# Kernel tuning notes

Hardware: AMD Instinct MI355X
Metric: run time of the kernel (lower is better)

Reference implementation:

```python
import math
import jax, jax.numpy as jnp
import numpy as np

B, S, HID = 2, 2048, 3072
NH, HD = 32, 96            # num_heads, head_dim; num_kv_heads == num_heads (n_rep = 1)
OP = NH * HD + 2 * (NH * HD)  # 9216


def _rope_tables(seq_len, head_dim, theta=10000.0):
    inv_freq = 1.0 / (theta ** (np.arange(0, head_dim, 2, dtype=np.float32) / head_dim))
    t = np.arange(seq_len, dtype=np.float32)
    freqs = np.outer(t, inv_freq)                      # [S, HD/2]
    emb = np.concatenate([freqs, freqs], axis=-1)      # [S, HD]
    return jnp.asarray(np.cos(emb)), jnp.asarray(np.sin(emb))


def setup_inputs() -> dict:
    key = jax.random.key(0)
    k1, k2, k3 = jax.random.split(key, 3)
    hidden_states = jax.random.normal(k1, (B, S, HID), dtype=jnp.float32)
    cos, sin = _rope_tables(S, HD)
    # additive causal mask [B, 1, S, S]
    neg = jnp.finfo(jnp.float32).min
    causal = jnp.where(jnp.tril(jnp.ones((S, S), dtype=bool)), 0.0, neg)
    attention_mask = jnp.broadcast_to(causal[None, None], (B, 1, S, S)).astype(jnp.float32)
    Wqkv = jax.random.normal(k2, (HID, OP), dtype=jnp.float32) * (HID ** -0.5)
    Wo = jax.random.normal(k3, (NH * HD, HID), dtype=jnp.float32) * ((NH * HD) ** -0.5)
    return {"hidden_states": hidden_states, "cos": cos, "sin": sin,
            "attention_mask": attention_mask, "Wqkv": Wqkv, "Wo": Wo}


def _rotate_half(x):
    x1, x2 = jnp.split(x, 2, axis=-1)
    return jnp.concatenate([-x2, x1], axis=-1)


def reference(hidden_states, cos, sin, attention_mask, Wqkv, Wo):
    bsz, q_len, _ = hidden_states.shape
    qkv = hidden_states @ Wqkv                                    # [B,S,OP]
    q, k, v = jnp.split(qkv, [NH * HD, 2 * NH * HD], axis=-1)
    # [B,S,H*D] -> [B,H,S,D]
    to_bhsd = lambda t: t.reshape(bsz, q_len, NH, HD).transpose(0, 2, 1, 3)
    q, k, v = to_bhsd(q), to_bhsd(k), to_bhsd(v)
    c = cos[None, None]                                           # [1,1,S,D]
    s = sin[None, None]
    q = q * c + _rotate_half(q) * s
    k = k * c + _rotate_half(k) * s
    # num_key_value_groups == 1, so repeat_kv is identity.
    scores = jnp.einsum('bhqd,bhkd->bhqk', q, k) / math.sqrt(HD)  # [B,H,S,S]
    scores = scores + attention_mask
    attn = jax.nn.softmax(scores.astype(jnp.float32), axis=-1).astype(v.dtype)
    # dropout p=0.0 / eval -> identity
    out = jnp.einsum('bhqk,bhkd->bhqd', attn, v)                  # [B,H,S,D]
    out = out.transpose(0, 2, 1, 3).reshape(bsz, q_len, NH * HD)
    return out @ Wo                                               # [B,S,HID]
```

## Files before the change

kernel.cpp:

```cpp
#include <hip/hip_runtime.h>

typedef __bf16  bf16x8 __attribute__((ext_vector_type(8)));
typedef float   f32x4  __attribute__((ext_vector_type(4)));
typedef float   f32x16 __attribute__((ext_vector_type(16)));
typedef short   i16x8  __attribute__((ext_vector_type(8)));
typedef unsigned short u16x4 __attribute__((ext_vector_type(4)));
typedef unsigned int   u32x4 __attribute__((ext_vector_type(4)));

__device__ __forceinline__ float bf2f(unsigned short u) {
    union { unsigned int i; float f; } v; v.i = ((unsigned int)u) << 16; return v.f;
}
__device__ __forceinline__ unsigned short f2bf(float f) {
    union { float f; unsigned int i; } v; v.f = f;
    unsigned int r = v.i + 0x7FFFu + ((v.i >> 16) & 1u);
    return (unsigned short)(r >> 16);
}
__device__ __forceinline__ unsigned packbf(float lo, float hi) {
    return (unsigned)f2bf(lo) | ((unsigned)f2bf(hi) << 16);
}
__device__ __forceinline__ void gload_lds16(const void* g, void* l) {
    __builtin_amdgcn_global_load_lds(
        (const __attribute__((address_space(1))) void*)g,
        (__attribute__((address_space(3))) void*)l, 16, 0, 0);
}
__device__ __forceinline__ void pswap(unsigned &x, unsigned &y) {
#if __has_builtin(__builtin_amdgcn_permlane32_swap)
    auto r = __builtin_amdgcn_permlane32_swap((int)x, (int)y, false, false);
    x = (unsigned)r[0]; y = (unsigned)r[1];
#else
    unsigned nx = (threadIdx.x & 32) ? (unsigned)__shfl_xor((int)y, 32) : x;
    unsigned ny = (threadIdx.x & 32) ? y : (unsigned)__shfl_xor((int)x, 32);
    x = nx; y = ny;
#endif
}
__device__ __forceinline__ float partner_f(float v, int hi) {
    unsigned x = __builtin_bit_cast(unsigned, v), y = x;
    pswap(x, y);
    return __builtin_bit_cast(float, hi ? x : y);
}

__global__ __launch_bounds__(256) void cast_f32_bf16(
    const float* __restrict__ in, unsigned short* __restrict__ out, int n8)
{
    int i = blockIdx.x * 256 + threadIdx.x;
    if (i >= n8) return;
    const f32x4* p = (const f32x4*)(in + (long)i * 8);
    f32x4 a = p[0], b = p[1];
    i16x8 o;
    o[0]=(short)f2bf(a[0]); o[1]=(short)f2bf(a[1]); o[2]=(short)f2bf(a[2]); o[3]=(short)f2bf(a[3]);
    o[4]=(short)f2bf(b[0]); o[5]=(short)f2bf(b[1]); o[6]=(short)f2bf(b[2]); o[7]=(short)f2bf(b[3]);
    *(i16x8*)(out + (long)i * 8) = o;
}

__global__ __launch_bounds__(256) void transpose_cast(
    const float* __restrict__ in, unsigned short* __restrict__ out, int R, int C)
{
    __shared__ float tile[64][65];
    int c0 = blockIdx.x * 64, r0 = blockIdx.y * 64;
    int tx = threadIdx.x & 63, ty = threadIdx.x >> 6;
#pragma unroll
    for (int i = 0; i < 64; i += 4)
        tile[ty + i][tx] = in[(long)(r0 + ty + i) * C + c0 + tx];
    __syncthreads();
#pragma unroll
    for (int i = 0; i < 64; i += 4)
        out[(long)(c0 + ty + i) * R + r0 + tx] = f2bf(tile[tx][ty + i]);
}

template <int MODE>
__global__ __launch_bounds__(256) void gemm_bt(
    const unsigned short* __restrict__ A, const unsigned short* __restrict__ B,
    int K, int N,
    unsigned short* __restrict__ Qo, unsigned short* __restrict__ Ko,
    unsigned short* __restrict__ Vo, float* __restrict__ Cf)
{
    __shared__ unsigned short Al[128 * 64];
    __shared__ unsigned short Bl[128 * 64];
    const int t = threadIdx.x;
    const int w = t >> 6, l = t & 63, lhi = l >> 4, llo = l & 15;
    const int m0 = blockIdx.x * 128, n0 = blockIdx.y * 128;
    const int wmo = (w >> 1) << 6, wno = (w & 1) << 6;

    const unsigned short* ag[4];
    const unsigned short* bg[4];
#pragma unroll
    for (int i = 0; i < 4; ++i) {
        int j = i * 256 + t;
        int row = j >> 3;
        int c = (j & 7) ^ (row & 7);
        ag[i] = A + (long)(m0 + row) * K + c * 8;
        bg[i] = B + (long)(n0 + row) * K + c * 8;
    }

    f32x4 acc[4][4] = {};
    const int nkt = K >> 6;
    for (int kt = 0; kt < nkt; ++kt) {
        __syncthreads();
#pragma unroll
        for (int i = 0; i < 4; ++i) {
            gload_lds16(ag[i] + kt * 64, &Al[(i * 256 + (w << 6)) * 8]);
            gload_lds16(bg[i] + kt * 64, &Bl[(i * 256 + (w << 6)) * 8]);
        }
        __syncthreads();
#pragma unroll
        for (int kf = 0; kf < 2; ++kf) {
            bf16x8 af[4], bfv[4];
#pragma unroll
            for (int mi = 0; mi < 4; ++mi) {
                int row = wmo + mi * 16 + llo;
                int cc = (kf * 4 + lhi) ^ (row & 7);
                af[mi] = __builtin_bit_cast(bf16x8, *(const i16x8*)&Al[row * 64 + cc * 8]);
            }
#pragma unroll
            for (int ni = 0; ni < 4; ++ni) {
                int row = wno + ni * 16 + llo;
                int cc = (kf * 4 + lhi) ^ (row & 7);
                bfv[ni] = __builtin_bit_cast(bf16x8, *(const i16x8*)&Bl[row * 64 + cc * 8]);
            }
#pragma unroll
            for (int mi = 0; mi < 4; ++mi)
#pragma unroll
                for (int ni = 0; ni < 4; ++ni)
                    acc[mi][ni] = __builtin_amdgcn_mfma_f32_16x16x32_bf16(
                        af[mi], bfv[ni], acc[mi][ni], 0, 0, 0);
        }
    }

#pragma unroll
    for (int mi = 0; mi < 4; ++mi) {
        int s0g = m0 + wmo + mi * 16 + (lhi << 2);
#pragma unroll
        for (int ni = 0; ni < 4; ++ni) {
            int gcol = n0 + wno + ni * 16 + llo;
            if (MODE == 1) {
#pragma unroll
                for (int r = 0; r < 4; ++r)
                    Cf[(long)(s0g + r) * N + gcol] = acc[mi][ni][r];
            } else {
                int seg = gcol / 3072;
                int cc2 = gcol - seg * 3072;
                int h = cc2 / 96, d = cc2 - h * 96;
                int b = s0g >> 11, s = s0g & 2047;
                long bh = (long)((b << 5) + h);
                if (seg == 2) {
                    u16x4 pv;
#pragma unroll
                    for (int r = 0; r < 4; ++r) pv[r] = f2bf(acc[mi][ni][r]);
                    *(u16x4*)(Vo + (bh * 96 + d) * 2048 + s) = pv;
                } else {
                    unsigned short* dst = seg ? Ko : Qo;
#pragma unroll
                    for (int r = 0; r < 4; ++r)
                        dst[(bh * 2048 + s + r) * 96 + d] = f2bf(acc[mi][ni][r]);
                }
            }
        }
    }
}

__global__ __launch_bounds__(256) void rope_kernel(
    unsigned short* __restrict__ Qb, unsigned short* __restrict__ Kb,
    const float* __restrict__ cosT, const float* __restrict__ sinT)
{
    int i = blockIdx.x * 256 + threadIdx.x;
    int d6 = i % 6;
    int sbh = i / 6;
    int s = sbh & 2047;
    long base = (long)sbh * 96 + d6 * 8;
    const f32x4* cp = (const f32x4*)(cosT + s * 96 + d6 * 8);
    const f32x4* sp = (const f32x4*)(sinT + s * 96 + d6 * 8);
    f32x4 c0 = cp[0], c1 = cp[1], s0 = sp[0], s1 = sp[1];
    float cv[8] = {c0[0],c0[1],c0[2],c0[3],c1[0],c1[1],c1[2],c1[3]};
    float sv[8] = {s0[0],s0[1],s0[2],s0[3],s1[0],s1[1],s1[2],s1[3]};
    i16x8 qlo = *(i16x8*)(Qb + base), qhi = *(i16x8*)(Qb + base + 48);
    i16x8 klo = *(i16x8*)(Kb + base), khi = *(i16x8*)(Kb + base + 48);
    i16x8 qlo2, qhi2, klo2, khi2;
#pragma unroll
    for (int j = 0; j < 8; ++j) {
        float ql = bf2f((unsigned short)qlo[j]), qh = bf2f((unsigned short)qhi[j]);
        float kl = bf2f((unsigned short)klo[j]), kh = bf2f((unsigned short)khi[j]);
        qlo2[j] = (short)f2bf(ql * cv[j] - qh * sv[j]);
        qhi2[j] = (short)f2bf(qh * cv[j] + ql * sv[j]);
        klo2[j] = (short)f2bf(kl * cv[j] - kh * sv[j]);
        khi2[j] = (short)f2bf(kh * cv[j] + kl * sv[j]);
    }
    *(i16x8*)(Qb + base) = qlo2; *(i16x8*)(Qb + base + 48) = qhi2;
    *(i16x8*)(Kb + base) = klo2; *(i16x8*)(Kb + base + 48) = khi2;
}

__global__ __launch_bounds__(256, 2) void attn_fwd(
    const unsigned short* __restrict__ Q, const unsigned short* __restrict__ Kt,
    const unsigned short* __restrict__ Vg, unsigned short* __restrict__ O)
{
    __shared__ __align__(16) unsigned short Kl[2][64 * 128];
    __shared__ __align__(16) unsigned short Vl[2][96 * 64];
    const int t = threadIdx.x;
    const int w = t >> 6, l = t & 63;
    const int l31 = l & 31, hi = l >> 5, l7 = l & 7;
    const int bh = blockIdx.x;
    const int qb = 7 - (int)blockIdx.y;
    const int q0b = qb << 8;
    const int nkv = 4 * qb + 4;
    const int kd = 4 * qb + w;
    constexpr float C2 = 0.14724450f;

    const unsigned short* Kg  = Kt + (long)bh * 2048 * 96;
    const unsigned short* Vgb = Vg + (long)bh * 96 * 2048;

#define STAGE_KV(buf, tile)                                                        \
    {                                                                              \
        _Pragma("unroll")                                                          \
        for (int i_ = 0; i_ < 4; ++i_) {                                           \
            int row_ = (w << 4) + (i_ << 2) + (l >> 4);                            \
            gload_lds16(Kg + ((long)(tile) * 64 + row_) * 96 +                     \
                            (((l & 15) ^ (row_ & 7)) << 3),                        \
                        &Kl[buf][((w << 4) + (i_ << 2)) << 7]);                    \
        }                                                                          \
        _Pragma("unroll")                                                          \
        for (int i_ = 0; i_ < 3; ++i_) {                                           \
            int row_ = w * 24 + (i_ << 3) + (l >> 3);                              \
            gload_lds16(Vgb + (long)row_ * 2048 + (tile) * 64 +                    \
                            ((l7 ^ (row_ & 7)) << 3),                              \
                        &Vl[buf][(w * 24 + (i_ << 3)) << 6]);                      \
        }                                                                          \
    }

    bf16x8 qf[2][6];
#pragma unroll
    for (int qs = 0; qs < 2; ++qs) {
        const unsigned short* qp =
            Q + ((long)bh * 2048 + q0b + (w << 6) + (qs << 5) + l31) * 96 + (hi << 3);
#pragma unroll
        for (int ks = 0; ks < 6; ++ks)
            qf[qs][ks] = __builtin_bit_cast(bf16x8, *(const i16x8*)(qp + ks * 16));
    }

    f32x16 oa[2][3] = {};
    float m_r[2] = {-1e30f, -1e30f};
    float l_r[2] = {0.f, 0.f};

    STAGE_KV(0, 0);
    __syncthreads();
    STAGE_KV(1, 1);

    for (int kt = 0; kt < nkv; ++kt) {
        const int cb = kt & 1;
        if (kt <= kd) {
            bf16x8 pf[2][4];
#pragma unroll
            for (int qs = 0; qs < 2; ++qs) {
                f32x16 s0 = {}, s1 = {};
#pragma unroll
                for (int ks = 0; ks < 6; ++ks) {
                    bf16x8 k0 = __builtin_bit_cast(bf16x8, *(const i16x8*)
                        &Kl[cb][(l31 << 7) + ((((ks << 1) + hi) ^ l7) << 3)]);
                    bf16x8 k1 = __builtin_bit_cast(bf16x8, *(const i16x8*)
                        &Kl[cb][((32 + l31) << 7) + ((((ks << 1) + hi) ^ l7) << 3)]);
                    s0 = __builtin_amdgcn_mfma_f32_32x32x16_bf16(k0, qf[qs][ks], s0, 0, 0, 0);
                    s1 = __builtin_amdgcn_mfma_f32_32x32x16_bf16(k1, qf[qs][ks], s1, 0, 0, 0);
                }
                if (kt == kd) {
                    const int ql = (qs << 5) + l31;
#pragma unroll
                    for (int r = 0; r < 16; ++r) {
                        int kvl = (r & 3) + ((r >> 2) << 3) + (hi << 2);
                        if (kvl > ql)      s0[r] = -1e30f;
                        if (kvl + 32 > ql) s1[r] = -1e30f;
                    }
                }
                float px = s0[0];
#pragma unroll
                for (int r = 1; r < 16; ++r) px = fmaxf(px, s0[r]);
#pragma unroll
                for (int r = 0; r < 16; ++r) px = fmaxf(px, s1[r]);
                px = fmaxf(px, partner_f(px, hi));
                if (__any(px > m_r[qs] + 54.0f)) {
                    float mnew = fmaxf(m_r[qs], px);
                    float scl = exp2f((m_r[qs] - mnew) * C2);
                    l_r[qs] *= scl;
#pragma unroll
                    for (int tt = 0; tt < 3; ++tt)
#pragma unroll
                        for (int r = 0; r < 16; ++r) oa[qs][tt][r] *= scl;
                    m_r[qs] = mnew;
                }
                const float mC = m_r[qs] * C2;
                f32x16 p0, p1;
                float ls = 0.f;
#pragma unroll
                for (int r = 0; r < 16; ++r) {
                    p0[r] = exp2f(fmaf(s0[r], C2, -mC));
                    p1[r] = exp2f(fmaf(s1[r], C2, -mC));
                    ls += p0[r] + p1[r];
                }
                l_r[qs] += ls;
#pragma unroll
                for (int s = 0; s < 4; ++s) {
                    const f32x16& pv = (s >= 2) ? p1 : p0;
                    const int bb = (s & 1) << 3;
                    unsigned d0 = packbf(pv[bb + 0], pv[bb + 1]);
                    unsigned d2 = packbf(pv[bb + 4], pv[bb + 5]);
                    pswap(d0, d2);
                    unsigned d1 = packbf(pv[bb + 2], pv[bb + 3]);
                    unsigned d3 = packbf(pv[bb + 6], pv[bb + 7]);
                    pswap(d1, d3);
                    pf[qs][s] = __builtin_bit_cast(bf16x8, (u32x4){d0, d1, d2, d3});
                }
            }
#pragma unroll
            for (int s = 0; s < 4; ++s) {
#pragma unroll
                for (int tt = 0; tt < 3; ++tt) {
                    bf16x8 vf = __builtin_bit_cast(bf16x8, *(const i16x8*)
                        &Vl[cb][((tt << 5) + l31) * 64 + ((((s << 1) + hi) ^ l7) << 3)]);
                    oa[0][tt] = __builtin_amdgcn_mfma_f32_32x32x16_bf16(vf, pf[0][s], oa[0][tt], 0, 0, 0);
                    oa[1][tt] = __builtin_amdgcn_mfma_f32_32x32x16_bf16(vf, pf[1][s], oa[1][tt], 0, 0, 0);
                }
            }
        }
        __syncthreads();
        if (kt + 2 < nkv) STAGE_KV(cb, kt + 2);
    }
#undef STAGE_KV

    const int b = bh >> 5, h = bh & 31;
#pragma unroll
    for (int qs = 0; qs < 2; ++qs) {
        float lt = l_r[qs] + partner_f(l_r[qs], hi);
        float inv = 1.0f / lt;
        const int qg = q0b + (w << 6) + (qs << 5) + l31;
        unsigned short* ob = O + ((long)(b * 2048 + qg)) * 3072 + h * 96;
#pragma unroll
        for (int tt = 0; tt < 3; ++tt)
#pragma unroll
            for (int qd = 0; qd < 4; ++qd) {
                u16x4 o4;
#pragma unroll
                for (int j = 0; j < 4; ++j)
                    o4[j] = f2bf(oa[qs][tt][(qd << 2) + j] * inv);
                *(u16x4*)(ob + (tt << 5) + (qd << 3) + (hi << 2)) = o4;
            }
    }
}

extern "C" void kernel_launch(void* const* d_in, const int* in_sizes, int n_in,
                              void* d_out, int out_size, void* d_ws, size_t ws_size,
                              hipStream_t stream) {
    const float* hidden = (const float*)d_in[0];
    const float* cosT   = (const float*)d_in[1];
    const float* sinT   = (const float*)d_in[2];
    const float* Wqkv   = (const float*)d_in[4];
    const float* Wo     = (const float*)d_in[5];
    float* out = (float*)d_out;

    char* ws = (char*)d_ws;
    unsigned short* Ah  = (unsigned short*)ws;
    unsigned short* WqT = (unsigned short*)(ws + 25165824);
    unsigned short* Qb  = (unsigned short*)(ws + 25165824 + 56623104);
    unsigned short* Kb  = Qb + 12582912;
    unsigned short* Vb  = Kb + 12582912;

    cast_f32_bf16<<<6144, 256, 0, stream>>>(hidden, Ah, 1572864);
    transpose_cast<<<dim3(144, 48), 256, 0, stream>>>(Wqkv, WqT, 3072, 9216);
    gemm_bt<0><<<dim3(32, 72), 256, 0, stream>>>(Ah, WqT, 3072, 9216, Qb, Kb, Vb, nullptr);
    transpose_cast<<<dim3(48, 48), 256, 0, stream>>>(Wo, WqT, 3072, 3072);
    rope_kernel<<<3072, 256, 0, stream>>>(Qb, Kb, cosT, sinT);
    attn_fwd<<<dim3(64, 8), 256, 0, stream>>>(Qb, Kb, Vb, Ah);
    gemm_bt<1><<<dim3(32, 24), 256, 0, stream>>>(Ah, WqT, 3072, 3072,
                                                 nullptr, nullptr, nullptr, out);
}
```

Before: 572.0 us.

## Pair causal query blocks per workgroup and triple-buffer KV with explicit waitcnt

Each attention workgroup now handles two query blocks (qb and 7-qb), so the causal work per block is balanced and the grid is halved to 256 blocks. KV staging moves from double to triple buffering, with manual vmcnt waits and raw barriers replacing __syncthreads, so two tiles are in flight while one is being computed. The QK loop is reordered so each K fragment feeds both query sub-tiles, and setprio raises priority around the MFMA sections. Occupancy is cut to one block per CU because of the larger LDS and register footprint, and the hand-written waitcnt counts depend on the exact number of loads STAGE_KV issues.

```diff
diff --git a/kernel.cpp b/kernel.cpp
--- a/kernel.cpp
+++ b/kernel.cpp
@@ -188,20 +188,16 @@
     *(i16x8*)(Kb + base) = klo2; *(i16x8*)(Kb + base + 48) = khi2;
 }
 
-__global__ __launch_bounds__(256, 2) void attn_fwd(
+__global__ __launch_bounds__(256, 1) void attn_fwd(
     const unsigned short* __restrict__ Q, const unsigned short* __restrict__ Kt,
     const unsigned short* __restrict__ Vg, unsigned short* __restrict__ O)
 {
-    __shared__ __align__(16) unsigned short Kl[2][64 * 128];
-    __shared__ __align__(16) unsigned short Vl[2][96 * 64];
+    __shared__ __align__(16) unsigned short Kl[3][64 * 128];
+    __shared__ __align__(16) unsigned short Vl[3][96 * 64];
     const int t = threadIdx.x;
     const int w = t >> 6, l = t & 63;
     const int l31 = l & 31, hi = l >> 5, l7 = l & 7;
     const int bh = blockIdx.x;
-    const int qb = 7 - (int)blockIdx.y;
-    const int q0b = qb << 8;
-    const int nkv = 4 * qb + 4;
-    const int kd = 4 * qb + w;
     constexpr float C2 = 0.14724450f;
 
     const unsigned short* Kg  = Kt + (long)bh * 2048 * 96;
@@ -225,122 +221,147 @@
         }                                                                          \
     }
 
-    bf16x8 qf[2][6];
-#pragma unroll
-    for (int qs = 0; qs < 2; ++qs) {
-        const unsigned short* qp =
-            Q + ((long)bh * 2048 + q0b + (w << 6) + (qs << 5) + l31) * 96 + (hi << 3);
-#pragma unroll
-        for (int ks = 0; ks < 6; ++ks)
-            qf[qs][ks] = __builtin_bit_cast(bf16x8, *(const i16x8*)(qp + ks * 16));
-    }
-
-    f32x16 oa[2][3] = {};
-    float m_r[2] = {-1e30f, -1e30f};
-    float l_r[2] = {0.f, 0.f};
-
-    STAGE_KV(0, 0);
-    __syncthreads();
-    STAGE_KV(1, 1);
-
-    for (int kt = 0; kt < nkv; ++kt) {
-        const int cb = kt & 1;
-        if (kt <= kd) {
-            bf16x8 pf[2][4];
-#pragma unroll
-            for (int qs = 0; qs < 2; ++qs) {
-                f32x16 s0 = {}, s1 = {};
+    const int b = bh >> 5, h = bh & 31;
+
+    for (int pass = 0; pass < 2; ++pass) {
+        const int qb = pass ? 7 - (int)blockIdx.y : (int)blockIdx.y;
+        const int q0b = qb << 8;
+        const int nkv = 4 * qb + 4;
+        const int kd = 4 * qb + w;
+
+        bf16x8 qf[2][6];
+#pragma unroll
+        for (int qs = 0; qs < 2; ++qs) {
+            const unsigned short* qp =
+                Q + ((long)bh * 2048 + q0b + (w << 6) + (qs << 5) + l31) * 96 + (hi << 3);
+#pragma unroll
+            for (int ks = 0; ks < 6; ++ks)
+                qf[qs][ks] = __builtin_bit_cast(bf16x8, *(const i16x8*)(qp + ks * 16));
+        }
+
+        f32x16 oa[2][3] = {};
+        float m_r[2] = {-1e30f, -1e30f};
+        float l_r[2] = {0.f, 0.f};
+
+        STAGE_KV(0, 0);
+        STAGE_KV(1, 1);
+        STAGE_KV(2, 2);
+
+        int cb = 0;
+        for (int kt = 0; kt < nkv; ++kt) {
+            const int rem = nkv - 1 - kt;
+            if (rem >= 2)      asm volatile("s_waitcnt vmcnt(14)" ::: "memory");
+            else if (rem == 1) asm volatile("s_waitcnt vmcnt(7)"  ::: "memory");
+            else               asm volatile("s_waitcnt vmcnt(0)"  ::: "memory");
+            __builtin_amdgcn_s_barrier();
+
+            if (kt <= kd) {
+                f32x16 s0[2] = {}, s1[2] = {};
+                __builtin_amdgcn_s_setprio(1);
 #pragma unroll
                 for (int ks = 0; ks < 6; ++ks) {
                     bf16x8 k0 = __builtin_bit_cast(bf16x8, *(const i16x8*)
                         &Kl[cb][(l31 << 7) + ((((ks << 1) + hi) ^ l7) << 3)]);
                     bf16x8 k1 = __builtin_bit_cast(bf16x8, *(const i16x8*)
                         &Kl[cb][((32 + l31) << 7) + ((((ks << 1) + hi) ^ l7) << 3)]);
-                    s0 = __builtin_amdgcn_mfma_f32_32x32x16_bf16(k0, qf[qs][ks], s0, 0, 0, 0);
-                    s1 = __builtin_amdgcn_mfma_f32_32x32x16_bf16(k1, qf[qs][ks], s1, 0, 0, 0);
-                }
-                if (kt == kd) {
-                    const int ql = (qs << 5) + l31;
+#pragma unroll
+                    for (int qs = 0; qs < 2; ++qs) {
+                        s0[qs] = __builtin_amdgcn_mfma_f32_32x32x16_bf16(k0, qf[qs][ks], s0[qs], 0, 0, 0);
+                        s1[qs] = __builtin_amdgcn_mfma_f32_32x32x16_bf16(k1, qf[qs][ks], s1[qs], 0, 0, 0);
+                    }
+                }
+                __builtin_amdgcn_s_setprio(0);
+
+                bf16x8 pf[2][4];
+#pragma unroll
+                for (int qs = 0; qs < 2; ++qs) {
+                    if (kt == kd) {
+                        const int ql = (qs << 5) + l31;
+#pragma unroll
+                        for (int r = 0; r < 16; ++r) {
+                            int kvl = (r & 3) + ((r >> 2) << 3) + (hi << 2);
+                            if (kvl > ql)      s0[qs][r] = -1e30f;
+                            if (kvl + 32 > ql) s1[qs][r] = -1e30f;
+                        }
+                    }
+                    float px = s0[qs][0];
+#pragma unroll
+                    for (int r = 1; r < 16; ++r) px = fmaxf(px, s0[qs][r]);
+#pragma unroll
+                    for (int r = 0; r < 16; ++r) px = fmaxf(px, s1[qs][r]);
+                    px = fmaxf(px, partner_f(px, hi));
+                    if (__any(px > m_r[qs] + 54.0f)) {
+                        float mnew = fmaxf(m_r[qs], px);
+                        float scl = exp2f((m_r[qs] - mnew) * C2);
+                        l_r[qs] *= scl;
+#pragma unroll
+                        for (int tt = 0; tt < 3; ++tt)
+#pragma unroll
+                            for (int r = 0; r < 16; ++r) oa[qs][tt][r] *= scl;
+                        m_r[qs] = mnew;
+                    }
+                    const float mC = m_r[qs] * C2;
+                    f32x16 p0, p1;
+                    float ls = 0.f;
 #pragma unroll
                     for (int r = 0; r < 16; ++r) {
-                        int kvl = (r & 3) + ((r >> 2) << 3) + (hi << 2);
-                        if (kvl > ql)      s0[r] = -1e30f;
-                        if (kvl + 32 > ql) s1[r] = -1e30f;
-                    }
-                }
-                float px = s0[0];
-#pragma unroll
-                for (int r = 1; r < 16; ++r) px = fmaxf(px, s0[r]);
-#pragma unroll
-                for (int r = 0; r < 16; ++r) px = fmaxf(px, s1[r]);
-                px = fmaxf(px, partner_f(px, hi));
-                if (__any(px > m_r[qs] + 54.0f)) {
-                    float mnew = fmaxf(m_r[qs], px);
-                    float scl = exp2f((m_r[qs] - mnew) * C2);
-                    l_r[qs] *= scl;
-#pragma unroll
-                    for (int tt = 0; tt < 3; ++tt)
-#pragma unroll
-                        for (int r = 0; r < 16; ++r) oa[qs][tt][r] *= scl;
-                    m_r[qs] = mnew;
-                }
-                const float mC = m_r[qs] * C2;
-                f32x16 p0, p1;
-                float ls = 0.f;
-#pragma unroll
-                for (int r = 0; r < 16; ++r) {
-                    p0[r] = exp2f(fmaf(s0[r], C2, -mC));
-                    p1[r] = exp2f(fmaf(s1[r], C2, -mC));
-                    ls += p0[r] + p1[r];
-                }
-                l_r[qs] += ls;
+                        p0[r] = exp2f(fmaf(s0[qs][r], C2, -mC));
+                        p1[r] = exp2f(fmaf(s1[qs][r], C2, -mC));
+                        ls += p0[r] + p1[r];
+                    }
+                    l_r[qs] += ls;
+#pragma unroll
+                    for (int s = 0; s < 4; ++s) {
+                        const f32x16& pv = (s >= 2) ? p1 : p0;
+                        const int bb = (s & 1) << 3;
+                        unsigned d0 = packbf(pv[bb + 0], pv[bb + 1]);
+                        unsigned d2 = packbf(pv[bb + 4], pv[bb + 5]);
+                        pswap(d0, d2);
+                        unsigned d1 = packbf(pv[bb + 2], pv[bb + 3]);
+                        unsigned d3 = packbf(pv[bb + 6], pv[bb + 7]);
+                        pswap(d1, d3);
+                        pf[qs][s] = __builtin_bit_cast(bf16x8, (u32x4){d0, d1, d2, d3});
+                    }
+                }
+                __builtin_amdgcn_s_setprio(1);
 #pragma unroll
                 for (int s = 0; s < 4; ++s) {
-                    const f32x16& pv = (s >= 2) ? p1 : p0;
-                    const int bb = (s & 1) << 3;
-                    unsigned d0 = packbf(pv[bb + 0], pv[bb + 1]);
-                    unsigned d2 = packbf(pv[bb + 4], pv[bb + 5]);
-                    pswap(d0, d2);
-                    unsigned d1 = packbf(pv[bb + 2], pv[bb + 3]);
-                    unsigned d3 = packbf(pv[bb + 6], pv[bb + 7]);
-                    pswap(d1, d3);
-                    pf[qs][s] = __builtin_bit_cast(bf16x8, (u32x4){d0, d1, d2, d3});
-                }
+#pragma unroll
+                    for (int tt = 0; tt < 3; ++tt) {
+                        bf16x8 vf = __builtin_bit_cast(bf16x8, *(const i16x8*)
+                            &Vl[cb][((tt << 5) + l31) * 64 + ((((s << 1) + hi) ^ l7) << 3)]);
+                        oa[0][tt] = __builtin_amdgcn_mfma_f32_32x32x16_bf16(vf, pf[0][s], oa[0][tt], 0, 0, 0);
+                        oa[1][tt] = __builtin_amdgcn_mfma_f32_32x32x16_bf16(vf, pf[1][s], oa[1][tt], 0, 0, 0);
+                    }
+                }
+                __builtin_amdgcn_s_setprio(0);
             }
-#pragma unroll
-            for (int s = 0; s < 4; ++s) {
-#pragma unroll
-                for (int tt = 0; tt < 3; ++tt) {
-                    bf16x8 vf = __builtin_bit_cast(bf16x8, *(const i16x8*)
-                        &Vl[cb][((tt << 5) + l31) * 64 + ((((s << 1) + hi) ^ l7) << 3)]);
-                    oa[0][tt] = __builtin_amdgcn_mfma_f32_32x32x16_bf16(vf, pf[0][s], oa[0][tt], 0, 0, 0);
-                    oa[1][tt] = __builtin_amdgcn_mfma_f32_32x32x16_bf16(vf, pf[1][s], oa[1][tt], 0, 0, 0);
-                }
-            }
-        }
-        __syncthreads();
-        if (kt + 2 < nkv) STAGE_KV(cb, kt + 2);
+
+            asm volatile("s_waitcnt lgkmcnt(0)" ::: "memory");
+            __builtin_amdgcn_s_barrier();
+            if (kt + 3 < nkv) STAGE_KV(cb, kt + 3);
+            cb = (cb == 2) ? 0 : cb + 1;
+        }
+
+#pragma unroll
+        for (int qs = 0; qs < 2; ++qs) {
+            float lt = l_r[qs] + partner_f(l_r[qs], hi);
+            float inv = 1.0f / lt;
+            const int qg = q0b + (w << 6) + (qs << 5) + l31;
+            unsigned short* ob = O + ((long)(b * 2048 + qg)) * 3072 + h * 96;
+#pragma unroll
+            for (int tt = 0; tt < 3; ++tt)
+#pragma unroll
+                for (int qd = 0; qd < 4; ++qd) {
+                    u16x4 o4;
+#pragma unroll
+                    for (int j = 0; j < 4; ++j)
+                        o4[j] = f2bf(oa[qs][tt][(qd << 2) + j] * inv);
+                    *(u16x4*)(ob + (tt << 5) + (qd << 3) + (hi << 2)) = o4;
+                }
+        }
     }
 #undef STAGE_KV
-
-    const int b = bh >> 5, h = bh & 31;
-#pragma unroll
-    for (int qs = 0; qs < 2; ++qs) {
-        float lt = l_r[qs] + partner_f(l_r[qs], hi);
-        float inv = 1.0f / lt;
-        const int qg = q0b + (w << 6) + (qs << 5) + l31;
-        unsigned short* ob = O + ((long)(b * 2048 + qg)) * 3072 + h * 96;
-#pragma unroll
-        for (int tt = 0; tt < 3; ++tt)
-#pragma unroll
-            for (int qd = 0; qd < 4; ++qd) {
-                u16x4 o4;
-#pragma unroll
-                for (int j = 0; j < 4; ++j)
-                    o4[j] = f2bf(oa[qs][tt][(qd << 2) + j] * inv);
-                *(u16x4*)(ob + (tt << 5) + (qd << 3) + (hi << 2)) = o4;
-            }
-    }
 }
 
 extern "C" void kernel_launch(void* const* d_in, const int* in_sizes, int n_in,
@@ -365,7 +386,7 @@
     gemm_bt<0><<<dim3(32, 72), 256, 0, stream>>>(Ah, WqT, 3072, 9216, Qb, Kb, Vb, nullptr);
     transpose_cast<<<dim3(48, 48), 256, 0, stream>>>(Wo, WqT, 3072, 3072);
     rope_kernel<<<3072, 256, 0, stream>>>(Qb, Kb, cosT, sinT);
-    attn_fwd<<<dim3(64, 8), 256, 0, stream>>>(Qb, Kb, Vb, Ah);
+    attn_fwd<<<dim3(64, 4), 256, 0, stream>>>(Qb, Kb, Vb, Ah);
     gemm_bt<1><<<dim3(32, 24), 256, 0, stream>>>(Ah, WqT, 3072, 3072,
                                                  nullptr, nullptr, nullptr, out);
 }
```

Result: faster. 547.4 us (-4.3%).
